# Optimization experiments

Hardware: AMD Instinct MI355X
Metric: run time of the kernel (lower is better)

## Reference

```python
import jax, jax.numpy as jnp
import numpy as np

# Hardcoded output spatial dims from the original call() (EEG: 62 channels x 375 timesteps)
H, W = 62, 375
N = 16            # batch size
P = H * W         # 23250 patch positions (x_1 dim of cal_val)
KFLAT = 1 * 5 * 25  # flattened kernel size = prod(output_dimension)
F = 64            # number of filters


def setup_inputs() -> dict:
    key = jax.random.key(0)
    k1, k2, k3 = jax.random.split(key, 3)
    x = jax.random.normal(k1, (N, P, KFLAT), dtype=jnp.float32)            # cal_val
    encoding_vector = jax.random.normal(k2, (P, KFLAT), dtype=jnp.float32)
    w = jax.random.normal(k3, (1, 5, 25, F), dtype=jnp.float32) * 0.05      # learned kernel
    return {"x": x, "encoding_vector": encoding_vector, "w": w}


def reference(x, encoding_vector, w):
    n, p, k = x.shape
    f = w.shape[-1]
    # build() flattens each filter: Kernel[j] = w[:, :, :, j].reshape(-1)  -> [F, kflat]
    kernel = jnp.moveaxis(w, 3, 0).reshape(f, k)
    # Original per-filter loop computes sum_k (kernel[f,k] + enc[p,k]) * x[n,p,k]
    # without materializing the tiled [N, P, kflat] kernel tensor:
    # out[f,n,p] = <kernel[f], x[n,p]> + <enc[p], x[n,p]>
    out_fnp = jnp.einsum('fk,npk->fnp', kernel, x) \
        + jnp.einsum('pk,npk->np', encoding_vector, x)[None, :, :]
    # Faithful final reshape of stacked [F, N, P] tensor into [N, F, H, W]
    return out_fnp.reshape(n, f, H, W)
```

## Files before the change

kernel.cpp:

```cpp
#include <hip/hip_runtime.h>


#define P_    23250u
#define K_    125
#define F_    64
#define M_TOT 372000
#define BM    64
#define NBLK  ((M_TOT + BM - 1) / BM)
#define TSTR  68

typedef __bf16 bf16;
typedef __bf16 bf16x4 __attribute__((ext_vector_type(4)));
typedef __bf16 bf16x8 __attribute__((ext_vector_type(8)));
typedef float  f32x4  __attribute__((ext_vector_type(4)));
typedef float  f32x4u __attribute__((ext_vector_type(4), aligned(4)));

__global__ __launch_bounds__(256, 1)
void prep_wfrag(const float* __restrict__ w, bf16* __restrict__ wfrag)
{
    const int tid = threadIdx.x;
    const int f  = ((tid >> 6) << 4) | (tid & 15);
    const int kg = (tid >> 4) & 3;
    #pragma unroll
    for (int ks = 0; ks < 4; ++ks) {
        bf16x8 fr;
        #pragma unroll
        for (int j = 0; j < 8; ++j) {
            const int k = ks * 32 + kg * 8 + j;
            fr[j] = (bf16)((k < K_) ? w[k * F_ + f] : 0.0f);
        }
        *(bf16x8*)(wfrag + tid * 32 + ks * 8) = fr;
    }
}

__global__ __launch_bounds__(256, 8)
void eegconv_kernel(const float* __restrict__ x,
                    const float* __restrict__ enc,
                    const bf16* __restrict__ wfrag,
                    float* __restrict__ out)
{
    __shared__ __attribute__((aligned(16))) char raw[F_ * TSTR * 4];
    __shared__ __attribute__((aligned(16))) float srow[BM];

    const int tid  = threadIdx.x;
    const int lane = tid & 63;
    const int wv   = tid >> 6;
    const int fl   = lane & 15;
    const int kg   = lane >> 4;
    const int r0   = blockIdx.x * BM;

    bf16x8 kf[4];
    {
        const bf16x8* wf = (const bf16x8*)(wfrag + tid * 32);
        #pragma unroll
        for (int ks = 0; ks < 4; ++ks) kf[ks] = wf[ks];
    }

    bf16* xt = (bf16*)raw;
    {
        const int row = tid >> 2;
        const int t4  = tid & 3;
        int gi = r0 + row;
        if (gi >= M_TOT) gi = 0;
        const float* xr = x   + (size_t)gi * K_;
        const float* er = enc + (size_t)((unsigned)gi % P_) * K_;
        char* lbase = (char*)xt + row * 256;
        const int sw = (row & 7) << 4;
        float part = 0.0f;

        #pragma unroll
        for (int u = 0; u < 8; ++u) {
            const int c = u * 4 + t4;
            f32x4 xv, ev;
            if (c < 31) {
                xv = (f32x4)*(const f32x4u*)(xr + c * 4);
                ev = (f32x4)*(const f32x4u*)(er + c * 4);
            } else {
                xv = f32x4{xr[124], 0.f, 0.f, 0.f};
                ev = f32x4{er[124], 0.f, 0.f, 0.f};
            }
            part += ev.x * xv.x + ev.y * xv.y + ev.z * xv.z + ev.w * xv.w;
            bf16x4 bv;
            bv[0] = (bf16)xv.x; bv[1] = (bf16)xv.y; bv[2] = (bf16)xv.z; bv[3] = (bf16)xv.w;
            *(bf16x4*)(lbase + ((c * 8) ^ sw)) = bv;
        }
        part += __shfl_xor(part, 1);
        part += __shfl_xor(part, 2);
        if (t4 == 0) srow[row] = part;
    }
    __syncthreads();

    f32x4 acc[4];
    #pragma unroll
    for (int t = 0; t < 4; ++t) acc[t] = f32x4{0.f, 0.f, 0.f, 0.f};

    #pragma unroll
    for (int t = 0; t < 4; ++t) {
        const int il = t * 16 + fl;
        const char* rbase = (const char*)xt + il * 256;
        const int sw = (il & 7) << 4;
        #pragma unroll
        for (int ks = 0; ks < 4; ++ks) {
            const bf16x8 av = *(const bf16x8*)(rbase + ((ks * 64 + kg * 16) ^ sw));
            acc[t] = __builtin_amdgcn_mfma_f32_16x16x32_bf16(av, kf[ks], acc[t], 0, 0, 0);
        }
    }
    __syncthreads();

    float* tr = (float*)raw;
    {
        const int f = wv * 16 + fl;
        #pragma unroll
        for (int t = 0; t < 4; ++t) {
            const int i0 = t * 16 + kg * 4;
            *(f32x4*)(tr + f * TSTR + i0) = acc[t];
        }
    }
    __syncthreads();

    {
        const int m8 = tid & 7;
        const int fg = tid >> 3;
        #pragma unroll
        for (int p = 0; p < 2; ++p) {
            const int f = p * 32 + fg;
            const float* src = tr + f * TSTR;
            const size_t ob = (size_t)f * M_TOT + r0;
            #pragma unroll
            for (int h = 0; h < 2; ++h) {
                const int ii = h * 32 + m8 * 4;
                if (r0 + ii < M_TOT) {
                    f32x4 v  = *(const f32x4*)(src + ii);
                    const f32x4 sv = *(const f32x4*)(srow + ii);
                    v.x += sv.x; v.y += sv.y; v.z += sv.z; v.w += sv.w;
                    *(f32x4*)(out + ob + ii) = v;
                }
            }
        }
    }
}

extern "C" void kernel_launch(void* const* d_in, const int* in_sizes, int n_in,
                              void* d_out, int out_size, void* d_ws, size_t ws_size,
                              hipStream_t stream)
{
    const float* x   = (const float*)d_in[0];
    const float* enc = (const float*)d_in[1];
    const float* w   = (const float*)d_in[2];
    float* out = (float*)d_out;
    bf16* wfrag = (bf16*)d_ws;
    prep_wfrag<<<1, 256, 0, stream>>>(w, wfrag);
    eegconv_kernel<<<NBLK, 256, 0, stream>>>(x, enc, wfrag, out);
}
```

Baseline: 355.0 us.

## Remap blocks so batch members sharing a patch tile run together on one XCD

Workgroups are re-indexed as (patch tile, batch index), and the 16 batch members of each patch tile are placed consecutively within the same XCD chunk via blockIdx&7 swizzling. The intent is for the encoding_vector rows to be reused from L2 across the batch instead of being refetched from memory. Tiles no longer cross batch boundaries, which adds a partial-tile scalar store path and slightly more blocks (some rows padded). The launch-bounds occupancy hint is also lowered from 8 to 4.

```diff
diff --git a/kernel.cpp b/kernel.cpp
--- a/kernel.cpp
+++ b/kernel.cpp
@@ -1,12 +1,14 @@
 #include <hip/hip_runtime.h>
 
 
-#define P_    23250u
+#define P_    23250
 #define K_    125
 #define F_    64
+#define N_    16
 #define M_TOT 372000
-#define BM    64
-#define NBLK  ((M_TOT + BM - 1) / BM)
+#define NPT   364
+#define NWG   (NPT * N_)
+#define CPX   (NWG / 8)
 #define TSTR  68
 
 typedef __bf16 bf16;
@@ -33,21 +35,25 @@
     }
 }
 
-__global__ __launch_bounds__(256, 8)
+__global__ __launch_bounds__(256, 4)
 void eegconv_kernel(const float* __restrict__ x,
                     const float* __restrict__ enc,
                     const bf16* __restrict__ wfrag,
                     float* __restrict__ out)
 {
     __shared__ __attribute__((aligned(16))) char raw[F_ * TSTR * 4];
-    __shared__ __attribute__((aligned(16))) float srow[BM];
+    __shared__ __attribute__((aligned(16))) float srow[64];
 
     const int tid  = threadIdx.x;
     const int lane = tid & 63;
     const int wv   = tid >> 6;
     const int fl   = lane & 15;
     const int kg   = lane >> 4;
-    const int r0   = blockIdx.x * BM;
+
+    const int wgid  = (blockIdx.x & 7) * CPX + (blockIdx.x >> 3);
+    const int ptile = wgid >> 4;
+    const int n     = wgid & 15;
+    const int p0    = ptile * 64;
 
     bf16x8 kf[4];
     {
@@ -60,10 +66,10 @@
     {
         const int row = tid >> 2;
         const int t4  = tid & 3;
-        int gi = r0 + row;
-        if (gi >= M_TOT) gi = 0;
-        const float* xr = x   + (size_t)gi * K_;
-        const float* er = enc + (size_t)((unsigned)gi % P_) * K_;
+        const int p   = p0 + row;
+        const int pe  = (p < P_) ? p : 0;
+        const float* xr = x   + (size_t)(n * P_ + pe) * K_;
+        const float* er = enc + (size_t)pe * K_;
         char* lbase = (char*)xt + row * 256;
         const int sw = (row & 7) << 4;
         float part = 0.0f;
@@ -121,19 +127,24 @@
     {
         const int m8 = tid & 7;
         const int fg = tid >> 3;
+        const bool full = (p0 + 64 <= P_);
         #pragma unroll
-        for (int p = 0; p < 2; ++p) {
-            const int f = p * 32 + fg;
+        for (int pp = 0; pp < 2; ++pp) {
+            const int f = pp * 32 + fg;
             const float* src = tr + f * TSTR;
-            const size_t ob = (size_t)f * M_TOT + r0;
+            float* ob = out + (size_t)f * M_TOT + (size_t)n * P_ + p0;
             #pragma unroll
             for (int h = 0; h < 2; ++h) {
                 const int ii = h * 32 + m8 * 4;
-                if (r0 + ii < M_TOT) {
-                    f32x4 v  = *(const f32x4*)(src + ii);
-                    const f32x4 sv = *(const f32x4*)(srow + ii);
-                    v.x += sv.x; v.y += sv.y; v.z += sv.z; v.w += sv.w;
-                    *(f32x4*)(out + ob + ii) = v;
+                f32x4 v  = *(const f32x4*)(src + ii);
+                const f32x4 sv = *(const f32x4*)(srow + ii);
+                v.x += sv.x; v.y += sv.y; v.z += sv.z; v.w += sv.w;
+                if (full) {
+                    *(f32x4u*)(ob + ii) = v;
+                } else {
+                    #pragma unroll
+                    for (int e = 0; e < 4; ++e)
+                        if (p0 + ii + e < P_) ob[ii + e] = v[e];
                 }
             }
         }
@@ -150,5 +161,5 @@
     float* out = (float*)d_out;
     bf16* wfrag = (bf16*)d_ws;
     prep_wfrag<<<1, 256, 0, stream>>>(w, wfrag);
-    eegconv_kernel<<<NBLK, 256, 0, stream>>>(x, enc, wfrag, out);
+    eegconv_kernel<<<NWG, 256, 0, stream>>>(x, enc, wfrag, out);
 }
```

Measured after the change: 325.7 us. 8.3% less time.

## Loop over batch per position tile with double-buffered async LDS staging

Applied to the files above, without the earlier changes.

Each block now owns a tile of 32 patch positions and iterates over all 16 batch items. The encoding rows are staged into LDS once and reused across the batch. Each x tile is pulled straight into LDS with global_load_lds, double-buffered so the next batch item's load overlaps the current compute and stores. The grid shrinks to 727 blocks at lower occupancy, which trades launch-level parallelism for reuse and overlap. The change also risks bank conflicts from scalar LDS reads at a 500-byte row stride.

```diff
diff --git a/kernel.cpp b/kernel.cpp
--- a/kernel.cpp
+++ b/kernel.cpp
@@ -1,16 +1,19 @@
 #include <hip/hip_runtime.h>
+#include <stdint.h>
 
 
-#define P_    23250u
+#define P_    23250
 #define K_    125
 #define F_    64
+#define NN    16
 #define M_TOT 372000
-#define BM    64
-#define NBLK  ((M_TOT + BM - 1) / BM)
-#define TSTR  68
+#define BM    32
+#define NPT   727
+#define TILEB 16384
+#define XBYTES ((size_t)M_TOT * 500)
+#define EBYTES ((size_t)P_ * 500)
 
 typedef __bf16 bf16;
-typedef __bf16 bf16x4 __attribute__((ext_vector_type(4)));
 typedef __bf16 bf16x8 __attribute__((ext_vector_type(8)));
 typedef float  f32x4  __attribute__((ext_vector_type(4)));
 typedef float  f32x4u __attribute__((ext_vector_type(4), aligned(4)));
@@ -33,13 +36,27 @@
     }
 }
 
-__global__ __launch_bounds__(256, 8)
+#define STAGE16K(GBASE, GLIM, LDSB)                                            \
+    do {                                                                       \
+        _Pragma("unroll")                                                      \
+        for (int r_ = 0; r_ < 4; ++r_) {                                       \
+            const char* g_ = (GBASE) + r_ * 4096 + tid * 16;                   \
+            if (g_ > (GLIM)) g_ = (GLIM);                                      \
+            __builtin_amdgcn_global_load_lds(                                  \
+                (const __attribute__((address_space(1))) uint32_t*)g_,         \
+                (__attribute__((address_space(3))) uint32_t*)((LDSB) + r_ * 4096 + wvoff), \
+                16, 0, 0);                                                     \
+        }                                                                      \
+    } while (0)
+
+__global__ __launch_bounds__(256, 3)
 void eegconv_kernel(const float* __restrict__ x,
                     const float* __restrict__ enc,
                     const bf16* __restrict__ wfrag,
                     float* __restrict__ out)
 {
-    __shared__ __attribute__((aligned(16))) char raw[F_ * TSTR * 4];
+    __shared__ __attribute__((aligned(16))) char encT[TILEB];
+    __shared__ __attribute__((aligned(16))) char xT[2][TILEB];
     __shared__ __attribute__((aligned(16))) float srow[BM];
 
     const int tid  = threadIdx.x;
@@ -47,96 +64,110 @@
     const int wv   = tid >> 6;
     const int fl   = lane & 15;
     const int kg   = lane >> 4;
-    const int r0   = blockIdx.x * BM;
+    const int wvoff = wv << 10;
+
+    const int ptile = blockIdx.x;
+    const int p0    = ptile * BM;
 
     bf16x8 kf[4];
     {
-        const bf16x8* wf = (const bf16x8*)(wfrag + tid * 32);
+        const bf16x8* wfp = (const bf16x8*)(wfrag + tid * 32);
         #pragma unroll
-        for (int ks = 0; ks < 4; ++ks) kf[ks] = wf[ks];
+        for (int ks = 0; ks < 4; ++ks) kf[ks] = wfp[ks];
     }
 
-    bf16* xt = (bf16*)raw;
-    {
-        const int row = tid >> 2;
-        const int t4  = tid & 3;
-        int gi = r0 + row;
-        if (gi >= M_TOT) gi = 0;
-        const float* xr = x   + (size_t)gi * K_;
-        const float* er = enc + (size_t)((unsigned)gi % P_) * K_;
-        char* lbase = (char*)xt + row * 256;
-        const int sw = (row & 7) << 4;
-        float part = 0.0f;
-
-        #pragma unroll
-        for (int u = 0; u < 8; ++u) {
-            const int c = u * 4 + t4;
-            f32x4 xv, ev;
-            if (c < 31) {
-                xv = (f32x4)*(const f32x4u*)(xr + c * 4);
-                ev = (f32x4)*(const f32x4u*)(er + c * 4);
-            } else {
-                xv = f32x4{xr[124], 0.f, 0.f, 0.f};
-                ev = f32x4{er[124], 0.f, 0.f, 0.f};
-            }
-            part += ev.x * xv.x + ev.y * xv.y + ev.z * xv.z + ev.w * xv.w;
-            bf16x4 bv;
-            bv[0] = (bf16)xv.x; bv[1] = (bf16)xv.y; bv[2] = (bf16)xv.z; bv[3] = (bf16)xv.w;
-            *(bf16x4*)(lbase + ((c * 8) ^ sw)) = bv;
-        }
-        part += __shfl_xor(part, 1);
-        part += __shfl_xor(part, 2);
-        if (t4 == 0) srow[row] = part;
-    }
-    __syncthreads();
-
-    f32x4 acc[4];
-    #pragma unroll
-    for (int t = 0; t < 4; ++t) acc[t] = f32x4{0.f, 0.f, 0.f, 0.f};
-
-    #pragma unroll
-    for (int t = 0; t < 4; ++t) {
-        const int il = t * 16 + fl;
-        const char* rbase = (const char*)xt + il * 256;
-        const int sw = (il & 7) << 4;
-        #pragma unroll
-        for (int ks = 0; ks < 4; ++ks) {
-            const bf16x8 av = *(const bf16x8*)(rbase + ((ks * 64 + kg * 16) ^ sw));
-            acc[t] = __builtin_amdgcn_mfma_f32_16x16x32_bf16(av, kf[ks], acc[t], 0, 0, 0);
-        }
-    }
-    __syncthreads();
-
-    float* tr = (float*)raw;
-    {
-        const int f = wv * 16 + fl;
-        #pragma unroll
-        for (int t = 0; t < 4; ++t) {
-            const int i0 = t * 16 + kg * 4;
-            *(f32x4*)(tr + f * TSTR + i0) = acc[t];
-        }
-    }
-    __syncthreads();
+    const char* xg   = (const char*)x;
+    const char* eg   = (const char*)enc;
+    const char* xlim = xg + (XBYTES - 16);
+    const char* elim = eg + ((EBYTES - 16) & ~(size_t)15);
 
     {
-        const int m8 = tid & 7;
-        const int fg = tid >> 3;
+        const char* eb = eg + (size_t)p0 * 500;
+        STAGE16K(eb, elim, encT);
+        const size_t xb0 = (size_t)p0 * 500;
+        const char* ab = xg + (xb0 & ~(size_t)15);
+        STAGE16K(ab, xlim, xT[0]);
+        asm volatile("s_waitcnt vmcnt(0)" ::: "memory");
+        __builtin_amdgcn_s_barrier();
+        __builtin_amdgcn_sched_barrier(0);
+    }
+
+    const size_t xstride = (size_t)P_ * 500;
+    float* const outb = out + (size_t)(wv * 16 + fl) * M_TOT + p0;
+    const bool fullt = (p0 + BM <= P_);
+
+    for (int n = 0; n < NN; ++n) {
+        const int cur  = n & 1;
+        const int xoff = (n & 1) << 3;
+
+        if (n + 1 < NN) {
+            const size_t xb = (size_t)(n + 1) * xstride + (size_t)p0 * 500;
+            const char* ab = xg + (xb & ~(size_t)15);
+            STAGE16K(ab, xlim, xT[cur ^ 1]);
+        }
+
+        {
+            const int row = tid >> 3, t8 = tid & 7;
+            const float* xr = (const float*)(xT[cur] + xoff + row * 500);
+            const float* er = (const float*)(encT + row * 500);
+            float part = 0.f;
+            #pragma unroll
+            for (int u = 0; u < 4; ++u) {
+                const int c = u * 8 + t8;
+                const int b = c * 4;
+                float x0 = xr[b], x1 = xr[b+1], x2 = xr[b+2], x3 = xr[b+3];
+                const float e0 = er[b], e1 = er[b+1], e2 = er[b+2], e3 = er[b+3];
+                if (c == 31) { x1 = 0.f; x2 = 0.f; x3 = 0.f; }
+                part += e0*x0 + e1*x1 + e2*x2 + e3*x3;
+            }
+            part += __shfl_xor(part, 1);
+            part += __shfl_xor(part, 2);
+            part += __shfl_xor(part, 4);
+            if (t8 == 0) srow[row] = part;
+        }
+        asm volatile("s_waitcnt lgkmcnt(0)" ::: "memory");
+        __builtin_amdgcn_s_barrier();
+        __builtin_amdgcn_sched_barrier(0);
+
+        f32x4 acc0 = {0.f,0.f,0.f,0.f}, acc1 = {0.f,0.f,0.f,0.f};
         #pragma unroll
-        for (int p = 0; p < 2; ++p) {
-            const int f = p * 32 + fg;
-            const float* src = tr + f * TSTR;
-            const size_t ob = (size_t)f * M_TOT + r0;
+        for (int t = 0; t < 2; ++t) {
+            const int il = t * 16 + fl;
+            const float* xrow = (const float*)(xT[cur] + xoff + il * 500);
             #pragma unroll
-            for (int h = 0; h < 2; ++h) {
-                const int ii = h * 32 + m8 * 4;
-                if (r0 + ii < M_TOT) {
-                    f32x4 v  = *(const f32x4*)(src + ii);
-                    const f32x4 sv = *(const f32x4*)(srow + ii);
-                    v.x += sv.x; v.y += sv.y; v.z += sv.z; v.w += sv.w;
-                    *(f32x4*)(out + ob + ii) = v;
+            for (int ks = 0; ks < 4; ++ks) {
+                const int kb = ks * 32 + kg * 8;
+                bf16x8 af;
+                #pragma unroll
+                for (int j = 0; j < 8; ++j) af[j] = (bf16)xrow[kb + j];
+                if (t == 0) acc0 = __builtin_amdgcn_mfma_f32_16x16x32_bf16(af, kf[ks], acc0, 0, 0, 0);
+                else        acc1 = __builtin_amdgcn_mfma_f32_16x16x32_bf16(af, kf[ks], acc1, 0, 0, 0);
+            }
+        }
+
+        {
+            float* ob = outb + (size_t)n * P_;
+            #pragma unroll
+            for (int t = 0; t < 2; ++t) {
+                const int i0 = t * 16 + kg * 4;
+                const f32x4 sv = *(const f32x4*)&srow[i0];
+                const f32x4 a = t ? acc1 : acc0;
+                f32x4 v;
+                v.x = a.x + sv.x; v.y = a.y + sv.y;
+                v.z = a.z + sv.z; v.w = a.w + sv.w;
+                if (fullt) {
+                    *(f32x4u*)(ob + i0) = v;
+                } else {
+                    #pragma unroll
+                    for (int e = 0; e < 4; ++e)
+                        if (p0 + i0 + e < P_) ob[i0 + e] = v[e];
                 }
             }
         }
+
+        __builtin_amdgcn_s_barrier();
+        asm volatile("s_waitcnt vmcnt(2)" ::: "memory");
+        __builtin_amdgcn_sched_barrier(0);
     }
 }
 
@@ -150,5 +181,5 @@
     float* out = (float*)d_out;
     bf16* wfrag = (bf16*)d_ws;
     prep_wfrag<<<1, 256, 0, stream>>>(w, wfrag);
-    eegconv_kernel<<<NBLK, 256, 0, stream>>>(x, enc, wfrag, out);
+    eegconv_kernel<<<NPT, 256, 0, stream>>>(x, enc, wfrag, out);
 }
```

After: 335.0 us. 5.7% less time.
